# Optimization experiments

Hardware: AMD Instinct MI355X
Metric: run time of the kernel (lower is better)

## Reference

```python
import jax, jax.numpy as jnp
import numpy as np

HEADS, DIM_HEAD = 16, 64
MAX_FREQ = 256.0

def axial_freqs(H, W):
    # rotary_embedding_torch, freqs_for='pixel': base freqs = linspace(1, max_freq/2, dim//2)*pi
    # with rotary dim = DIM_HEAD//2 per axis, so DIM_HEAD//4 base frequencies per axis.
    nf = DIM_HEAD // 4
    base = jnp.linspace(1.0, MAX_FREQ / 2.0, nf) * jnp.pi
    def per_axis(n):
        pos = jnp.linspace(-1.0, 1.0, n)              # pixel positions in [-1, 1]
        fr = pos[:, None] * base[None, :]             # (n, DIM_HEAD//4)
        return jnp.repeat(fr, 2, axis=-1)             # (n, DIM_HEAD//2), interleaved repeat
    fh = jnp.broadcast_to(per_axis(H)[:, None, :], (H, W, DIM_HEAD // 2))
    fw = jnp.broadcast_to(per_axis(W)[None, :, :], (H, W, DIM_HEAD // 2))
    return jnp.concatenate([fh, fw], axis=-1)         # (H, W, DIM_HEAD)

def rotate_half(x):
    # interleaved-pair rotation: (x0,x1,x2,x3,...) -> (-x1,x0,-x3,x2,...)
    x2 = x.reshape(x.shape[:-1] + (-1, 2))
    a, b = x2[..., 0], x2[..., 1]
    return jnp.stack([-b, a], axis=-1).reshape(x.shape)

def apply_rot(freqs, t):
    return t * jnp.cos(freqs) + rotate_half(t) * jnp.sin(freqs)

def setup_inputs() -> dict:
    key = jax.random.key(0)
    ks = jax.random.split(key, 6)
    B, T, H, W, dim = 1, 2, 16, 16, 1024
    inner = HEADS * DIM_HEAD
    S, K = H * W, 144
    x = jax.random.normal(ks[0], (B, T, H, W, dim), jnp.float32)
    w_qkv = jax.random.normal(ks[1], (3 * inner, dim), jnp.float32) * (dim ** -0.5)
    w_out = jax.random.normal(ks[2], (dim, inner), jnp.float32) * (inner ** -0.5)
    b_out = jnp.zeros((dim,), jnp.float32)
    out_not_top_k = jax.random.normal(ks[3], (B * T, HEADS, S, DIM_HEAD), jnp.float32) * 0.02
    top_k_indices = jax.random.randint(ks[4], (B * T, HEADS, S, K), 0, S, jnp.int32)
    return {"x": x, "w_qkv": w_qkv, "w_out": w_out, "b_out": b_out,
            "out_not_top_k": out_not_top_k, "top_k_indices": top_k_indices}

def reference(x, w_qkv, w_out, b_out, out_not_top_k, top_k_indices):
    B, T, H, W, dim = x.shape
    inner = HEADS * DIM_HEAD
    S = H * W
    # qkv projection (torch Linear: y = x @ W^T)
    qkv = jnp.einsum('bthwc,oc->bthwo', x, w_qkv)
    q, k, v = jnp.split(qkv, 3, axis=-1)

    def to_grid(t):
        t = t.reshape(B * T, H, W, HEADS, DIM_HEAD)
        return jnp.transpose(t, (0, 3, 1, 2, 4))       # (BT, h, H, W, d)
    q, k, v = map(to_grid, (q, k, v))

    freqs = axial_freqs(H, W)                          # (H, W, d), broadcasts over (BT, h)
    q = apply_rot(freqs, q)
    k = apply_rot(freqs, k)

    q = q.reshape(B * T, HEADS, S, DIM_HEAD)
    k = k.reshape(B * T, HEADS, S, DIM_HEAD)
    v = v.reshape(B * T, HEADS, S, DIM_HEAD)

    scale = DIM_HEAD ** -0.5
    idx = top_k_indices[..., None]                      # (BT, h, S, K, 1)
    # per-query gather of top-k keys/values: out[b,h,s,k,:] = k[b,h,idx[b,h,s,k],:]
    k_g = jnp.take_along_axis(k[:, :, None, :, :], idx, axis=3)  # (BT, h, S, K, d)
    v_g = jnp.take_along_axis(v[:, :, None, :, :], idx, axis=3)

    scores = jnp.einsum('bhsd,bhskd->bhsk', q, k_g) * scale
    probs = jax.nn.softmax(scores, axis=-1)
    out_top = jnp.einsum('bhsk,bhskd->bhsd', probs, v_g)

    out = out_top + out_not_top_k                       # (BT, h, S, d)
    out = jnp.transpose(out.reshape(B * T, HEADS, H, W, DIM_HEAD), (0, 2, 3, 1, 4))
    out = out.reshape(B, T, H, W, inner)
    return jnp.einsum('bthwi,oi->bthwo', out, w_out) + b_out
```

## Files before the change

### kernel.cpp

```cpp
#include <hip/hip_runtime.h>
#include <hip/hip_bf16.h>
#include <math.h>

#define BTN   2
#define NH    16
#define SEQ   256
#define DH    64
#define DIMF  1024
#define KTOP  144
#define QT    16
#define PI_F  3.14159265358979323846f

typedef _Float16 half8 __attribute__((ext_vector_type(8)));
typedef _Float16 half4v __attribute__((ext_vector_type(4)));
typedef float f32x4 __attribute__((ext_vector_type(4)));

#define GLDS(src, dst) __builtin_amdgcn_global_load_lds( \
        (const __attribute__((address_space(1))) void*)(src), \
        (__attribute__((address_space(3))) void*)(dst), 16, 0, 0)

#define N0Q (524288 / 4)
#define N1Q (3145728 / 4)
#define N2Q (1048576 / 4)
__global__ __launch_bounds__(256)
void cvt3_kernel(const float* __restrict__ a, const float* __restrict__ b,
                 const float* __restrict__ c,
                 _Float16* __restrict__ da, _Float16* __restrict__ db,
                 _Float16* __restrict__ dc)
{
    int q = blockIdx.x * 256 + threadIdx.x;
    const float* s; _Float16* d; int off;
    if (q < N0Q)            { s = a; d = da; off = q; }
    else if (q < N0Q + N1Q) { s = b; d = db; off = q - N0Q; }
    else                    { s = c; d = dc; off = q - (N0Q + N1Q); }
    const float4 v = *(const float4*)(s + (size_t)off * 4);
    half4v h;
    h[0] = (_Float16)v.x; h[1] = (_Float16)v.y;
    h[2] = (_Float16)v.z; h[3] = (_Float16)v.w;
    *(half4v*)(d + (size_t)off * 4) = h;
}

template <int MODE>
__global__ __launch_bounds__(256)
void gemm32_kernel(const _Float16* __restrict__ A, const _Float16* __restrict__ B,
                   int N,
                   _Float16* __restrict__ qb, _Float16* __restrict__ kb,
                   _Float16* __restrict__ vb,
                   const float* __restrict__ bias, float* __restrict__ out)
{
    __shared__ __align__(16) _Float16 As[32 * 64];
    __shared__ __align__(16) _Float16 Bs[64 * 64];

    const int Kd   = DIMF;
    const int tid  = threadIdx.x;
    const int wave = tid >> 6;
    const int lane = tid & 63;
    const int row0 = blockIdx.y * 32;
    const int col0 = blockIdx.x * 64;
    const int rl = lane >> 3;
    const int cl = lane & 7;

    f32x4 acc[2] = {};

    for (int kt = 0; kt < Kd; kt += 64) {
        __syncthreads();
        {
            const int rA = wave * 8 + rl;
            GLDS(A + (size_t)(row0 + rA) * Kd + kt + ((cl ^ (rA & 7)) * 8),
                 As + wave * 8 * 64);
        }
#pragma unroll
        for (int h = 0; h < 2; ++h) {
            const int rB = wave * 16 + h * 8 + rl;
            GLDS(B + (size_t)(col0 + rB) * Kd + kt + ((cl ^ (rB & 7)) * 8),
                 Bs + (wave * 16 + h * 8) * 64);
        }
        __syncthreads();

#pragma unroll
        for (int kh = 0; kh < 2; ++kh) {
            const int g = kh * 4 + (lane >> 4);
            half8 a[2], b;
#pragma unroll
            for (int i = 0; i < 2; ++i) {
                const int ra = i * 16 + (lane & 15);
                a[i] = *(const half8*)(As + ra * 64 + ((g ^ (ra & 7)) * 8));
            }
            const int rb = wave * 16 + (lane & 15);
            b = *(const half8*)(Bs + rb * 64 + ((g ^ (rb & 7)) * 8));
#pragma unroll
            for (int i = 0; i < 2; ++i)
                acc[i] = __builtin_amdgcn_mfma_f32_16x16x32_f16(a[i], b, acc[i], 0, 0, 0);
        }
    }

    if (MODE == 0) {
#pragma unroll
        for (int i = 0; i < 2; ++i) {
#pragma unroll
            for (int reg = 0; reg < 4; ++reg) {
                const int r  = row0 + i * 16 + (lane >> 4) * 4 + reg;
                const int bt = r >> 8;
                const int s  = r & 255;
                const int hh = s >> 4;
                const int ww = s & 15;
                const float v     = acc[i][reg];
                const float other = __shfl_xor(v, 1);
                const int n    = col0 + wave * 16 + (lane & 15);
                const int sec  = n >> 10;
                const int oi   = n & 1023;
                const int head = oi >> 6;
                const int d    = oi & 63;
                if (sec == 2) {
                    vb[(((size_t)(bt * NH + head)) * DH + d) * SEQ + s] = (_Float16)v;
                } else {
                    const int de  = d & ~1;
                    const int j2  = (de < 32) ? (de >> 1) : ((de - 32) >> 1);
                    const float pos = (de < 32) ? (-1.f + hh * (2.f / 15.f))
                                                : (-1.f + ww * (2.f / 15.f));
                    const float f  = pos * (PI_F * (1.f + j2 * (127.f / 15.f)));
                    const float cf = __cosf(f), sf = __sinf(f);
                    const float res = (d & 1) ? (v * cf + other * sf)
                                              : (v * cf - other * sf);
                    _Float16* dp = (sec == 0) ? qb : kb;
                    dp[(((size_t)(bt * NH + head)) * SEQ + s) * DH + d] = (_Float16)res;
                }
            }
        }
    } else {
#pragma unroll
        for (int i = 0; i < 2; ++i)
#pragma unroll
            for (int reg = 0; reg < 4; ++reg) {
                const int r = row0 + i * 16 + (lane >> 4) * 4 + reg;
                const int n = col0 + wave * 16 + (lane & 15);
                out[(size_t)r * N + n] = acc[i][reg] + bias[n];
            }
    }
}

__global__ __launch_bounds__(256)
void attn_reg16_kernel(const _Float16* __restrict__ qh, const _Float16* __restrict__ kh,
                       const _Float16* __restrict__ vt, const int* __restrict__ topk,
                       const float* __restrict__ ontk, _Float16* __restrict__ attnh)
{
    __shared__ __align__(16) float Ps[QT * 256];

    const int tid  = threadIdx.x;
    const int w    = tid >> 6;
    const int lane = tid & 63;
    const int bid  = blockIdx.x;
    const int bt   = bid >> 8;
    const int head = (bid >> 4) & 15;
    const int s0   = (bid & 15) * QT;
    const int bh   = bt * NH + head;

    half8 aq[2], bk[2][4];
#pragma unroll
    for (int kk = 0; kk < 2; ++kk) {
        const int c8 = (kk * 4 + (lane >> 4)) * 8;
        aq[kk] = *(const half8*)(qh + ((size_t)bh * SEQ + s0 + (lane & 15)) * DH + c8);
#pragma unroll
        for (int j = 0; j < 4; ++j)
            bk[kk][j] = *(const half8*)(kh + ((size_t)bh * SEQ + w * 64 + j * 16 + (lane & 15)) * DH + c8);
    }
    int ki0[4], ki1[4], ki2[4];
#pragma unroll
    for (int qq = 0; qq < 4; ++qq) {
        const int* idxp = topk + ((size_t)bh * SEQ + s0 + w * 4 + qq) * KTOP;
        ki0[qq] = idxp[lane];
        ki1[qq] = idxp[lane + 64];
        ki2[qq] = idxp[(lane < 16) ? (lane + 128) : lane];
    }
    half8 bv[8];
    {
        const _Float16* vrow = vt + ((size_t)bh * DH + w * 16 + (lane & 15)) * SEQ
                                  + (lane >> 4) * 8;
#pragma unroll
        for (int ks = 0; ks < 8; ++ks)
            bv[ks] = *(const half8*)(vrow + ks * 32);
    }
    float on[4];
#pragma unroll
    for (int reg = 0; reg < 4; ++reg) {
        const int row = (lane >> 4) * 4 + reg;
        on[reg] = ontk[((size_t)bh * SEQ + s0 + row) * DH + w * 16 + (lane & 15)];
    }

    f32x4 acc[4] = {};
#pragma unroll
    for (int kk = 0; kk < 2; ++kk)
#pragma unroll
        for (int j = 0; j < 4; ++j)
            acc[j] = __builtin_amdgcn_mfma_f32_16x16x32_f16(aq[kk], bk[kk][j], acc[j], 0, 0, 0);
#pragma unroll
    for (int j = 0; j < 4; ++j)
#pragma unroll
        for (int reg = 0; reg < 4; ++reg) {
            const int row = (lane >> 4) * 4 + reg;
            const int col = w * 64 + j * 16 + (lane & 15);
            Ps[row * 256 + (col ^ ((row & 7) << 2))] = acc[j][reg];
        }
    __syncthreads();

#pragma unroll
    for (int qq = 0; qq < 4; ++qq) {
        const int q  = w * 4 + qq;
        const int sw = (q & 7) << 2;
        float* prow  = Ps + q * 256;
        const float sv0 = prow[ki0[qq] ^ sw] * 0.125f;
        const float sv1 = prow[ki1[qq] ^ sw] * 0.125f;
        const float sv2 = (lane < 16) ? prow[ki2[qq] ^ sw] * 0.125f : -1e30f;
        float m = fmaxf(fmaxf(sv0, sv1), sv2);
#pragma unroll
        for (int off = 32; off; off >>= 1) m = fmaxf(m, __shfl_xor(m, off));
        const float e0 = __expf(sv0 - m);
        const float e1 = __expf(sv1 - m);
        const float e2 = (lane < 16) ? __expf(sv2 - m) : 0.f;
        float z = e0 + e1 + e2;
#pragma unroll
        for (int off = 32; off; off >>= 1) z += __shfl_xor(z, off);
        const float inv = 1.f / z;
#pragma unroll
        for (int c2 = 0; c2 < 4; ++c2) prow[lane + c2 * 64] = 0.f;
        atomicAdd(&prow[ki0[qq] ^ sw], e0 * inv);
        atomicAdd(&prow[ki1[qq] ^ sw], e1 * inv);
        if (lane < 16) atomicAdd(&prow[ki2[qq] ^ sw], e2 * inv);
    }
    __syncthreads();

    f32x4 oacc = {};
#pragma unroll
    for (int ks = 0; ks < 8; ++ks) {
        const int ra = lane & 15;
        const int b0 = ks * 32 + (lane >> 4) * 8;
        const int sw = (ra & 7) << 2;
        const float4 p0 = *(const float4*)(Ps + ra * 256 + (b0 ^ sw));
        const float4 p1 = *(const float4*)(Ps + ra * 256 + ((b0 + 4) ^ sw));
        half8 af;
        af[0] = (_Float16)p0.x; af[1] = (_Float16)p0.y;
        af[2] = (_Float16)p0.z; af[3] = (_Float16)p0.w;
        af[4] = (_Float16)p1.x; af[5] = (_Float16)p1.y;
        af[6] = (_Float16)p1.z; af[7] = (_Float16)p1.w;
        oacc = __builtin_amdgcn_mfma_f32_16x16x32_f16(af, bv[ks], oacc, 0, 0, 0);
    }
#pragma unroll
    for (int reg = 0; reg < 4; ++reg) {
        const int row = (lane >> 4) * 4 + reg;
        const int d   = w * 16 + (lane & 15);
        const int s   = s0 + row;
        attnh[((size_t)(bt * SEQ + s)) * DIMF + head * DH + d] = (_Float16)(oacc[reg] + on[reg]);
    }
}

extern "C" void kernel_launch(void* const* d_in, const int* in_sizes, int n_in,
                              void* d_out, int out_size, void* d_ws, size_t ws_size,
                              hipStream_t stream) {
    const float* x     = (const float*)d_in[0];
    const float* w_qkv = (const float*)d_in[1];
    const float* w_out = (const float*)d_in[2];
    const float* b_out = (const float*)d_in[3];
    const float* ontk  = (const float*)d_in[4];
    const int*   topk  = (const int*)d_in[5];
    float* out = (float*)d_out;

    const size_t QE = (size_t)BTN * NH * SEQ * DH;

    _Float16* xh    = (_Float16*)d_ws;
    _Float16* wqh   = xh + 524288;
    _Float16* woh   = wqh + 3145728;
    _Float16* attnh = woh + 1048576;
    _Float16* qhb   = attnh + QE;
    _Float16* khb   = qhb + QE;
    _Float16* vtb   = khb + QE;

    cvt3_kernel<<<(N0Q + N1Q + N2Q) / 256, 256, 0, stream>>>(x, w_qkv, w_out, xh, wqh, woh);

    gemm32_kernel<0><<<dim3(3072 / 64, 512 / 32), 256, 0, stream>>>(
        xh, wqh, 3072, qhb, khb, vtb, nullptr, nullptr);

    attn_reg16_kernel<<<BTN * NH * (SEQ / QT), 256, 0, stream>>>(
        qhb, khb, vtb, topk, ontk, attnh);

    gemm32_kernel<1><<<dim3(1024 / 64, 512 / 32), 256, 0, stream>>>(
        attnh, woh, 1024, nullptr, nullptr, nullptr, b_out, out);
}
```

Baseline: 46.44 us.

## Deepen GEMM K-tile to 128 and shrink output GEMM N-tile to 32

Both GEMMs now stage a 128-wide K slice per iteration using a 16-way XOR swizzle, which halves the number of barrier-separated load/compute rounds. The output projection uses a 32x32 tile, with each wave computing one 16x16 quadrant, so it launches twice as many blocks to fill more CUs on the small 512x1024 problem. The costs are more LDS per block and less reuse per block in the output GEMM.

```diff
diff --git a/kernel.cpp b/kernel.cpp
--- a/kernel.cpp
+++ b/kernel.cpp
@@ -42,55 +42,71 @@
 
 template <int MODE>
 __global__ __launch_bounds__(256)
-void gemm32_kernel(const _Float16* __restrict__ A, const _Float16* __restrict__ B,
-                   int N,
-                   _Float16* __restrict__ qb, _Float16* __restrict__ kb,
-                   _Float16* __restrict__ vb,
-                   const float* __restrict__ bias, float* __restrict__ out)
+void gemm_k128_kernel(const _Float16* __restrict__ A, const _Float16* __restrict__ B,
+                      int N,
+                      _Float16* __restrict__ qb, _Float16* __restrict__ kb,
+                      _Float16* __restrict__ vb,
+                      const float* __restrict__ bias, float* __restrict__ out)
 {
-    __shared__ __align__(16) _Float16 As[32 * 64];
-    __shared__ __align__(16) _Float16 Bs[64 * 64];
+    constexpr int BN = (MODE == 0) ? 64 : 32;
+    __shared__ __align__(16) _Float16 As[32 * 128];
+    __shared__ __align__(16) _Float16 Bs[BN * 128];
 
     const int Kd   = DIMF;
     const int tid  = threadIdx.x;
     const int wave = tid >> 6;
     const int lane = tid & 63;
     const int row0 = blockIdx.y * 32;
-    const int col0 = blockIdx.x * 64;
-    const int rl = lane >> 3;
-    const int cl = lane & 7;
+    const int col0 = blockIdx.x * BN;
+    const int rl4  = lane >> 4;
+    const int cl16 = lane & 15;
 
     f32x4 acc[2] = {};
 
-    for (int kt = 0; kt < Kd; kt += 64) {
+    for (int kt = 0; kt < 8; ++kt) {
         __syncthreads();
-        {
-            const int rA = wave * 8 + rl;
-            GLDS(A + (size_t)(row0 + rA) * Kd + kt + ((cl ^ (rA & 7)) * 8),
-                 As + wave * 8 * 64);
-        }
 #pragma unroll
         for (int h = 0; h < 2; ++h) {
-            const int rB = wave * 16 + h * 8 + rl;
-            GLDS(B + (size_t)(col0 + rB) * Kd + kt + ((cl ^ (rB & 7)) * 8),
-                 Bs + (wave * 16 + h * 8) * 64);
+            const int rA = wave * 8 + h * 4 + rl4;
+            GLDS(A + (size_t)(row0 + rA) * Kd + kt * 128 + ((cl16 ^ (rA & 15)) * 8),
+                 As + (wave * 8 + h * 4) * 128);
+        }
+        if (MODE == 0) {
+#pragma unroll
+            for (int h = 0; h < 4; ++h) {
+                const int rB = wave * 16 + h * 4 + rl4;
+                GLDS(B + (size_t)(col0 + rB) * Kd + kt * 128 + ((cl16 ^ (rB & 15)) * 8),
+                     Bs + (wave * 16 + h * 4) * 128);
+            }
+        } else {
+#pragma unroll
+            for (int h = 0; h < 2; ++h) {
+                const int rB = wave * 8 + h * 4 + rl4;
+                GLDS(B + (size_t)(col0 + rB) * Kd + kt * 128 + ((cl16 ^ (rB & 15)) * 8),
+                     Bs + (wave * 8 + h * 4) * 128);
+            }
         }
         __syncthreads();
 
 #pragma unroll
-        for (int kh = 0; kh < 2; ++kh) {
+        for (int kh = 0; kh < 4; ++kh) {
             const int g = kh * 4 + (lane >> 4);
-            half8 a[2], b;
-#pragma unroll
-            for (int i = 0; i < 2; ++i) {
-                const int ra = i * 16 + (lane & 15);
-                a[i] = *(const half8*)(As + ra * 64 + ((g ^ (ra & 7)) * 8));
+            if (MODE == 0) {
+                const int rb = wave * 16 + (lane & 15);
+                const half8 b = *(const half8*)(Bs + rb * 128 + ((g ^ (rb & 15)) * 8));
+#pragma unroll
+                for (int i = 0; i < 2; ++i) {
+                    const int ra = i * 16 + (lane & 15);
+                    const half8 a = *(const half8*)(As + ra * 128 + ((g ^ (ra & 15)) * 8));
+                    acc[i] = __builtin_amdgcn_mfma_f32_16x16x32_f16(a, b, acc[i], 0, 0, 0);
+                }
+            } else {
+                const int ra = (wave >> 1) * 16 + (lane & 15);
+                const int rb = (wave & 1) * 16 + (lane & 15);
+                const half8 a = *(const half8*)(As + ra * 128 + ((g ^ (ra & 15)) * 8));
+                const half8 b = *(const half8*)(Bs + rb * 128 + ((g ^ (rb & 15)) * 8));
+                acc[0] = __builtin_amdgcn_mfma_f32_16x16x32_f16(a, b, acc[0], 0, 0, 0);
             }
-            const int rb = wave * 16 + (lane & 15);
-            b = *(const half8*)(Bs + rb * 64 + ((g ^ (rb & 7)) * 8));
-#pragma unroll
-            for (int i = 0; i < 2; ++i)
-                acc[i] = __builtin_amdgcn_mfma_f32_16x16x32_f16(a[i], b, acc[i], 0, 0, 0);
         }
     }
 
@@ -129,13 +145,11 @@
         }
     } else {
 #pragma unroll
-        for (int i = 0; i < 2; ++i)
-#pragma unroll
-            for (int reg = 0; reg < 4; ++reg) {
-                const int r = row0 + i * 16 + (lane >> 4) * 4 + reg;
-                const int n = col0 + wave * 16 + (lane & 15);
-                out[(size_t)r * N + n] = acc[i][reg] + bias[n];
-            }
+        for (int reg = 0; reg < 4; ++reg) {
+            const int r = row0 + (wave >> 1) * 16 + (lane >> 4) * 4 + reg;
+            const int n = col0 + (wave & 1) * 16 + (lane & 15);
+            out[(size_t)r * N + n] = acc[0][reg] + bias[n];
+        }
     }
 }
 
@@ -276,12 +290,12 @@
 
     cvt3_kernel<<<(N0Q + N1Q + N2Q) / 256, 256, 0, stream>>>(x, w_qkv, w_out, xh, wqh, woh);
 
-    gemm32_kernel<0><<<dim3(3072 / 64, 512 / 32), 256, 0, stream>>>(
+    gemm_k128_kernel<0><<<dim3(3072 / 64, 512 / 32), 256, 0, stream>>>(
         xh, wqh, 3072, qhb, khb, vtb, nullptr, nullptr);
 
     attn_reg16_kernel<<<BTN * NH * (SEQ / QT), 256, 0, stream>>>(
         qhb, khb, vtb, topk, ontk, attnh);
 
-    gemm32_kernel<1><<<dim3(1024 / 64, 512 / 32), 256, 0, stream>>>(
+    gemm_k128_kernel<1><<<dim3(1024 / 32, 512 / 32), 256, 0, stream>>>(
         attnh, woh, 1024, nullptr, nullptr, nullptr, b_out, out);
 }
```

Measured after the change: 41.47 us. 1.12x faster.
